# Optimization experiments

Measured on AMD Instinct MI355X. Metric: run time of the kernel, lower is better.

The kernel has to match this reference:

```python
import jax, jax.numpy as jnp
import numpy as np

LOG2E = 1.4426950408889634  # 1/ln(2): kernel works in log2 space with exp2


def _mlstm_chunkwise_single(q, k, v, vecI, vecF, chunk_size):
    # q,k: [T,K]; v: [T,V]; vecI,vecF: [T] (log2-space gate preactivations)
    T, K = q.shape
    V = v.shape[-1]
    BT = chunk_size
    NT = T // BT
    scale = K ** -0.5
    dt = q.dtype

    qc = q.reshape(NT, BT, K)
    kc = k.reshape(NT, BT, K)
    vc = v.reshape(NT, BT, V)
    ic = vecI.reshape(NT, BT)
    fc = vecF.reshape(NT, BT)
    b = jnp.cumsum(fc, axis=1)            # within-chunk cumulative log2 forget (vecF in kernel)
    f_last = b[:, -1]                      # scaF_last
    g = ic + f_last[:, None] - b           # decay from each pos to chunk end (vecG)

    tri = jnp.tril(jnp.ones((BT, BT), dtype=bool))

    def step(carry, inp):
        C, n, m = carry                    # [K,V], [K], scalar running max
        qt, kt, vt, it, bt, gt, fl = inp
        # intra-chunk decay matrix D[t,s] = i[s] + b[t] - b[s] for s<=t
        D = it[None, :] + bt[:, None] - bt[None, :]
        D = jnp.where(tri, D, -jnp.inf)
        m_intra = jnp.max(D, axis=1)                      # [BT]
        m_total = jnp.maximum(bt + m, m_intra)            # matM_total
        S = (qt @ kt.T) * (scale * jnp.exp2(D - m_total[:, None]))
        q_sc = qt * (scale * jnp.exp2(bt + m - m_total))[:, None]
        h_num = q_sc @ C + S @ vt                          # [BT,V]
        denom = jnp.maximum(jnp.abs(q_sc @ n + S.sum(axis=1)), jnp.exp2(-m_total))
        h = h_num / denom[:, None]
        # cross-chunk matrix-state recurrence with log2 restabilization
        m_next = jnp.maximum(fl + m, jnp.max(gt))
        dec = jnp.exp2(fl + m - m_next)
        kdec = kt * jnp.exp2(gt - m_next)[:, None]         # [BT,K]
        C_next = C * dec + kdec.T @ vt
        n_next = n * dec + kdec.sum(axis=0)
        return (C_next, n_next, m_next), h

    C0 = jnp.zeros((K, V), dt)
    n0 = jnp.zeros((K,), dt)
    m0 = jnp.zeros((), dt)
    _, hs = jax.lax.scan(step, (C0, n0, m0), (qc, kc, vc, ic, b, g, f_last))
    return hs.reshape(T, V)


def setup_inputs() -> dict:
    key = jax.random.key(0)
    ks = jax.random.split(key, 5)
    B, H, T, D = 8, 8, 4096, 64
    q = jax.random.normal(ks[0], (B, H, T, D), dtype=jnp.float32)
    k = jax.random.normal(ks[1], (B, H, T, D), dtype=jnp.float32)
    v = jax.random.normal(ks[2], (B, H, T, D), dtype=jnp.float32)
    i = jax.random.normal(ks[3], (B, H, T), dtype=jnp.float32)
    f = jax.random.normal(ks[4], (B, H, T), dtype=jnp.float32)
    return {"q": q, "k": k, "v": v, "i": i, "f": f, "chunk_size": 64}


def reference(q, k, v, i, f, chunk_size):
    B, H, T, K = q.shape
    V = v.shape[-1]
    vecF = jax.nn.log_sigmoid(f) * LOG2E   # log2 sigmoid(f)
    vecI = i * LOG2E                       # input gate in log2 space
    BH = B * H
    fn = lambda qq, kk, vv, ii, ff: _mlstm_chunkwise_single(qq, kk, vv, ii, ff, chunk_size)
    h = jax.vmap(fn)(q.reshape(BH, T, K), k.reshape(BH, T, K), v.reshape(BH, T, V),
                     vecI.reshape(BH, T), vecF.reshape(BH, T))
    return h.reshape(B, H, T, V)
```

## Files before the change

kernel.cpp:

```cpp
#include <hip/hip_runtime.h>
#include <hip/hip_bf16.h>
#include <math.h>

#define LOG2E_F 1.4426950408889634f

static constexpr int BT = 64;
static constexpr int DK = 64;
static constexpr int DV = 64;
static constexpr float SCALE = 0.125f;
static constexpr int PAD = 72;

typedef unsigned short ushort_t;
typedef __attribute__((ext_vector_type(8))) short short8;
typedef __attribute__((ext_vector_type(4))) float f32x4;
typedef __attribute__((ext_vector_type(4))) ushort_t ushort4v;

#define MFMA16(a, b, c) __builtin_amdgcn_mfma_f32_16x16x32_bf16((a), (b), (c), 0, 0, 0)

__device__ __forceinline__ int SWZ(int a, int b){ return a * PAD + (b ^ (((a >> 3) & 3) << 3)); }
__device__ __forceinline__ int ZSW(int r, int c){ return r * PAD + (c ^ (((r >> 2) & 3) << 3)); }
__device__ __forceinline__ int LIN(int r, int c){ return r * PAD + c; }

__device__ __forceinline__ float logsig_log2e(float x){
    float l = (x >= 0.f) ? (-log1pf(expf(-x))) : (x - log1pf(expf(x)));
    return l * LOG2E_F;
}
__device__ __forceinline__ ushort_t f2bf(float x){
    unsigned u = __builtin_bit_cast(unsigned, x);
    unsigned r = u + 0x7FFFu + ((u >> 16) & 1u);
    return (ushort_t)(r >> 16);
}
__device__ __forceinline__ float bf2f(ushort_t u){
    return __builtin_bit_cast(float, ((unsigned)u) << 16);
}
__device__ __forceinline__ void split_bf(float x, ushort_t& h, ushort_t& l){
    h = f2bf(x);
    l = f2bf(x - bf2f(h));
}

__global__ __launch_bounds__(256, 4) void stageA_kernel(
    const float* __restrict__ kg, const float* __restrict__ vg,
    const float* __restrict__ ig, const float* __restrict__ fg,
    float* __restrict__ A_ws, float* __restrict__ nloc_ws,
    float* __restrict__ fl_ws, float* __restrict__ mloc_ws,
    int T, int NT)
{
    const int ct = blockIdx.x, s = blockIdx.y, tid = threadIdx.x;
    const int w = tid >> 6, lane = tid & 63, ln = lane & 15, quad = lane >> 4;
    const int q8 = quad * 8;

    __shared__ __align__(16) ushort_t kth[BT * PAD];
    __shared__ __align__(16) ushort_t ktl[BT * PAD];
    __shared__ __align__(16) ushort_t vth[BT * PAD];
    __shared__ __align__(16) ushort_t vtl[BT * PAD];
    __shared__ float gsc[BT];

    const size_t rowbase = (size_t)s * T + (size_t)ct * BT;
    const float* kc = kg + rowbase * DK;
    const float* vc = vg + rowbase * DV;

    float4 kr[4], vr[4];
    #pragma unroll
    for (int i = 0; i < 4; ++i){
        int idx = i * 1024 + tid * 4;
        kr[i] = *(const float4*)(kc + idx);
        vr[i] = *(const float4*)(vc + idx);
    }
    if (tid < 64){
        float b = logsig_log2e(fg[rowbase + tid]);
        #pragma unroll
        for (int off = 1; off < 64; off <<= 1){
            float y = __shfl_up(b, off);
            if (tid >= off) b += y;
        }
        float f_last = __shfl(b, 63);
        float a = ig[rowbase + tid] * LOG2E_F - b;
        float p = a;
        #pragma unroll
        for (int off = 32; off > 0; off >>= 1) p = fmaxf(p, __shfl_xor(p, off));
        gsc[tid] = exp2f(a - p);
        if (tid == 0){ fl_ws[s * NT + ct] = f_last; mloc_ws[s * NT + ct] = f_last + p; }
    }
    __syncthreads();
    #pragma unroll
    for (int i = 0; i < 4; ++i){
        int idx = i * 1024 + tid * 4;
        int r = idx >> 6, c0 = idx & 63;
        float g = gsc[r];
        float kv[4] = {kr[i].x * g, kr[i].y * g, kr[i].z * g, kr[i].w * g};
        float vv[4] = {vr[i].x, vr[i].y, vr[i].z, vr[i].w};
        #pragma unroll
        for (int j = 0; j < 4; ++j){
            ushort_t h, l;
            split_bf(kv[j], h, l); kth[SWZ(c0 + j, r)] = h; ktl[SWZ(c0 + j, r)] = l;
            split_bf(vv[j], h, l); vth[SWZ(c0 + j, r)] = h; vtl[SWZ(c0 + j, r)] = l;
        }
    }
    __syncthreads();

    const int m = 16 * w + ln;
    short8 ah0 = *(const short8*)&kth[SWZ(m, q8)];
    short8 ah1 = *(const short8*)&kth[SWZ(m, 32 + q8)];
    short8 al0 = *(const short8*)&ktl[SWZ(m, q8)];
    short8 al1 = *(const short8*)&ktl[SWZ(m, 32 + q8)];
    float* Ab = A_ws + (size_t)(s * NT + ct) * 4096;
    #pragma unroll
    for (int t = 0; t < 4; ++t){
        f32x4 acc = {0.f, 0.f, 0.f, 0.f};
        short8 bh0 = *(const short8*)&vth[SWZ(16 * t + ln, q8)];
        short8 bh1 = *(const short8*)&vth[SWZ(16 * t + ln, 32 + q8)];
        short8 bl0 = *(const short8*)&vtl[SWZ(16 * t + ln, q8)];
        short8 bl1 = *(const short8*)&vtl[SWZ(16 * t + ln, 32 + q8)];
        acc = MFMA16(ah0, bh0, acc);
        acc = MFMA16(ah1, bh1, acc);
        acc = MFMA16(ah0, bl0, acc);
        acc = MFMA16(ah1, bl1, acc);
        acc = MFMA16(al0, bh0, acc);
        acc = MFMA16(al1, bh1, acc);
        *(f32x4*)(Ab + ((16 * t + ln) << 6) + 16 * w + quad * 4) = acc;
    }
    {
        short8 ones;
        #pragma unroll
        for (int j = 0; j < 8; ++j) ones[j] = (short)0x3F80;
        f32x4 nacc = {0.f, 0.f, 0.f, 0.f};
        nacc = MFMA16(ah0, ones, nacc);
        nacc = MFMA16(ah1, ones, nacc);
        nacc = MFMA16(al0, ones, nacc);
        nacc = MFMA16(al1, ones, nacc);
        if (ln == 0){
            #pragma unroll
            for (int reg = 0; reg < 4; ++reg)
                nloc_ws[((size_t)(s * NT + ct)) * DK + 16 * w + quad * 4 + reg] = nacc[reg];
        }
    }
}

__global__ __launch_bounds__(256) void stageB_kernel(
    const float* __restrict__ A_ws, const float* __restrict__ nloc_ws,
    const float* __restrict__ fl_ws, const float* __restrict__ mloc_ws,
    float* __restrict__ Cws, float* __restrict__ nws, float* __restrict__ mws,
    int NT)
{
    const int vb = blockIdx.x, s = blockIdx.y, tid = threadIdx.x;
    __shared__ float decs[64], scs[64];

    if (tid < 64){
        float fl = fl_ws[s * NT + tid];
        float ml = mloc_ws[s * NT + tid];
        float F = fl, G = ml;
        #pragma unroll
        for (int off = 1; off < 64; off <<= 1){
            float Fp = __shfl_up(F, off);
            float Gp = __shfl_up(G, off);
            if (tid >= off){ G = fmaxf(Gp + F, G); F = Fp + F; }
        }
        float m_next = fmaxf(F, G);
        float m_cur  = __shfl_up(m_next, 1);
        if (tid == 0) m_cur = 0.f;
        decs[tid] = exp2f(fl + m_cur - m_next);
        scs[tid]  = exp2f(ml - m_next);
        if (vb == 0) mws[s * NT + tid] = m_cur;
    }
    __syncthreads();

    const size_t base = (size_t)s * NT * 4096 + (size_t)vb * 256 + tid;
    const float* Ab = A_ws + base;
    float*       Cb = Cws  + base;
    const bool do_n = (vb == 0) && (tid < 64);

    float C = 0.f, nreg = 0.f;
    float p[8], nl[8];
    #pragma unroll
    for (int i = 0; i < 8; ++i){ p[i] = Ab[(size_t)i * 4096]; nl[i] = 0.f; }
    if (do_n){
        #pragma unroll
        for (int i = 0; i < 8; ++i) nl[i] = nloc_ws[((size_t)(s * NT + i)) * DK + tid];
    }

    for (int t0 = 0; t0 < NT; t0 += 8){
        float qv[8], nq[8];
        const int tn = t0 + 8;
        #pragma unroll
        for (int i = 0; i < 8; ++i)
            qv[i] = (tn + i < NT) ? Ab[(size_t)(tn + i) * 4096] : 0.f;
        #pragma unroll
        for (int i = 0; i < 8; ++i) nq[i] = 0.f;
        if (do_n){
            #pragma unroll
            for (int i = 0; i < 8; ++i)
                if (tn + i < NT) nq[i] = nloc_ws[((size_t)(s * NT + tn + i)) * DK + tid];
        }
        #pragma unroll
        for (int i = 0; i < 8; ++i){
            const int t = t0 + i;
            Cb[(size_t)t * 4096] = C;
            if (do_n) nws[((size_t)(s * NT + t)) * DK + tid] = nreg;
            const float d = decs[t], sc = scs[t];
            C = C * d + p[i] * sc;
            if (do_n) nreg = nreg * d + nl[i] * sc;
        }
        #pragma unroll
        for (int i = 0; i < 8; ++i){ p[i] = qv[i]; nl[i] = nq[i]; }
    }
}

__global__ __launch_bounds__(256, 4) void pass2_kernel(
    const float* __restrict__ qg, const float* __restrict__ kg, const float* __restrict__ vg,
    const float* __restrict__ ig, const float* __restrict__ fg,
    const float* __restrict__ Cws, const float* __restrict__ nws, const float* __restrict__ mws,
    float* __restrict__ out, int T, int NT)
{
    const int ct = blockIdx.x, s = blockIdx.y, tid = threadIdx.x;
    const int w = tid >> 6, lane = tid & 63, ln = lane & 15, quad = lane >> 4;
    const int q8 = quad * 8;

    __shared__ __align__(16) ushort_t bufA[BT * PAD];
    __shared__ __align__(16) ushort_t bufB[BT * PAD];
    __shared__ __align__(16) ushort_t bufZ[BT * PAD];
    __shared__ __align__(16) ushort_t bufV[BT * PAD];
    __shared__ float colterm[BT], Mr[BT], rowfac[BT], dncl[BT];
    __shared__ float nsh[DK], qn[BT], rowsum[BT];

    const size_t rowbase = (size_t)s * T + (size_t)ct * BT;
    const float* qc = qg + rowbase * DK;
    const float* kc = kg + rowbase * DK;
    const float* vc = vg + rowbase * DV;
    const float* Cc = Cws + ((size_t)(s * NT + ct)) * 4096;
    const float* nc = nws + ((size_t)(s * NT + ct)) * DK;
    const float m   = mws[s * NT + ct];

    float4 kr4[4], vr[4];
    #pragma unroll
    for (int i = 0; i < 4; ++i){
        int idx = i * 1024 + tid * 4;
        kr4[i] = *(const float4*)(kc + idx);
        vr[i]  = *(const float4*)(vc + idx);
    }
    const float* qrow = qc + (16 * w + ln) * DK;
    float4 qf0 = *(const float4*)(qrow + q8);
    float4 qf1 = *(const float4*)(qrow + q8 + 4);
    float4 qf2 = *(const float4*)(qrow + 32 + q8);
    float4 qf3 = *(const float4*)(qrow + 32 + q8 + 4);
    float4 Cr[4];
    #pragma unroll
    for (int i = 0; i < 4; ++i)
        Cr[i] = *(const float4*)(Cc + i * 1024 + tid * 4);

    if (tid < 64){
        float b = logsig_log2e(fg[rowbase + tid]);
        #pragma unroll
        for (int off = 1; off < 64; off <<= 1){
            float y = __shfl_up(b, off);
            if (tid >= off) b += y;
        }
        float a = ig[rowbase + tid] * LOG2E_F - b;
        float p = a;
        #pragma unroll
        for (int off = 1; off < 64; off <<= 1){
            float y = __shfl_up(p, off);
            if (tid >= off) p = fmaxf(p, y);
        }
        float M = fmaxf(m, p);
        colterm[tid] = a;
        Mr[tid] = M;
        rowfac[tid] = SCALE * exp2f(m - M);
        dncl[tid] = exp2f(-(b + M));
        nsh[tid] = nc[tid];
    }
    #pragma unroll
    for (int i = 0; i < 4; ++i){
        int idx = i * 1024 + tid * 4;
        int r = idx >> 6, c0 = idx & 63;
        float kv[4] = {kr4[i].x, kr4[i].y, kr4[i].z, kr4[i].w};
        ushort4v kh4, kl4;
        #pragma unroll
        for (int j = 0; j < 4; ++j){
            ushort_t h, l;
            split_bf(kv[j], h, l); kh4[j] = h; kl4[j] = l;
        }
        *(ushort4v*)&bufA[SWZ(r, c0)] = kh4;
        *(ushort4v*)&bufB[SWZ(r, c0)] = kl4;
    }
    __syncthreads();

    const int mrow = 16 * w + ln;
    float a0[8] = {qf0.x, qf0.y, qf0.z, qf0.w, qf1.x, qf1.y, qf1.z, qf1.w};
    float a1[8] = {qf2.x, qf2.y, qf2.z, qf2.w, qf3.x, qf3.y, qf3.z, qf3.w};
    short8 ah0, al0, ah1, al1;
    #pragma unroll
    for (int j = 0; j < 8; ++j){
        ushort_t h, l;
        split_bf(a0[j], h, l); ah0[j] = (short)h; al0[j] = (short)l;
        split_bf(a1[j], h, l); ah1[j] = (short)h; al1[j] = (short)l;
    }
    {
        float p = 0.f;
        #pragma unroll
        for (int j = 0; j < 8; ++j){
            p = fmaf(a0[j], nsh[q8 + j], p);
            p = fmaf(a1[j], nsh[32 + q8 + j], p);
        }
        p += __shfl_xor(p, 16);
        p += __shfl_xor(p, 32);
        if (quad == 0) qn[mrow] = p;
    }
    #pragma unroll
    for (int i = 0; i < 4; ++i){
        int idx = i * 1024 + tid * 4;
        int r = idx >> 6, c0 = idx & 63;
        float vv[4] = {vr[i].x, vr[i].y, vr[i].z, vr[i].w};
        #pragma unroll
        for (int j = 0; j < 4; ++j) bufV[SWZ(c0 + j, r)] = f2bf(vv[j]);
    }

    f32x4 sacc[4];
    #pragma unroll
    for (int t = 0; t < 4; ++t){
        sacc[t] = (f32x4){0.f, 0.f, 0.f, 0.f};
        short8 bh0 = *(const short8*)&bufA[SWZ(16 * t + ln, q8)];
        short8 bh1 = *(const short8*)&bufA[SWZ(16 * t + ln, 32 + q8)];
        short8 bl0 = *(const short8*)&bufB[SWZ(16 * t + ln, q8)];
        short8 bl1 = *(const short8*)&bufB[SWZ(16 * t + ln, 32 + q8)];
        sacc[t] = MFMA16(ah0, bh0, sacc[t]);
        sacc[t] = MFMA16(ah1, bh1, sacc[t]);
        sacc[t] = MFMA16(ah0, bl0, sacc[t]);
        sacc[t] = MFMA16(ah1, bl1, sacc[t]);
        sacc[t] = MFMA16(al0, bh0, sacc[t]);
        sacc[t] = MFMA16(al1, bh1, sacc[t]);
    }
    {
        float rsum[4] = {0.f, 0.f, 0.f, 0.f};
        float Mrv[4];
        #pragma unroll
        for (int reg = 0; reg < 4; ++reg) Mrv[reg] = Mr[16 * w + quad * 4 + reg];
        #pragma unroll
        for (int t = 0; t < 4; ++t){
            int c = 16 * t + ln;
            float cterm = colterm[c];
            #pragma unroll
            for (int reg = 0; reg < 4; ++reg){
                int r = 16 * w + quad * 4 + reg;
                float vS = (c <= r) ? sacc[t][reg] * SCALE * exp2f(cterm - Mrv[reg]) : 0.f;
                bufZ[ZSW(r, c)] = f2bf(vS);
                rsum[reg] += vS;
            }
        }
        #pragma unroll
        for (int off = 1; off < 16; off <<= 1){
            #pragma unroll
            for (int reg = 0; reg < 4; ++reg) rsum[reg] += __shfl_xor(rsum[reg], off);
        }
        if (ln == 0){
            #pragma unroll
            for (int reg = 0; reg < 4; ++reg) rowsum[16 * w + quad * 4 + reg] = rsum[reg];
        }
    }
    __syncthreads();

    #pragma unroll
    for (int i = 0; i < 4; ++i){
        int idx = i * 1024 + tid * 4;
        int vrow = idx >> 6, k0 = idx & 63;
        float cv[4] = {Cr[i].x, Cr[i].y, Cr[i].z, Cr[i].w};
        ushort4v ch4, cl4;
        #pragma unroll
        for (int j = 0; j < 4; ++j){
            ushort_t h, l;
            split_bf(cv[j], h, l); ch4[j] = h; cl4[j] = l;
        }
        *(ushort4v*)&bufA[SWZ(vrow, k0)] = ch4;
        *(ushort4v*)&bufB[SWZ(vrow, k0)] = cl4;
    }
    __syncthreads();

    f32x4 acc[4];
    #pragma unroll
    for (int t = 0; t < 4; ++t){
        acc[t] = (f32x4){0.f, 0.f, 0.f, 0.f};
        short8 bh0 = *(const short8*)&bufA[SWZ(16 * t + ln, q8)];
        short8 bh1 = *(const short8*)&bufA[SWZ(16 * t + ln, 32 + q8)];
        short8 bl0 = *(const short8*)&bufB[SWZ(16 * t + ln, q8)];
        short8 bl1 = *(const short8*)&bufB[SWZ(16 * t + ln, 32 + q8)];
        acc[t] = MFMA16(ah0, bh0, acc[t]);
        acc[t] = MFMA16(ah1, bh1, acc[t]);
        acc[t] = MFMA16(ah0, bl0, acc[t]);
        acc[t] = MFMA16(ah1, bl1, acc[t]);
        acc[t] = MFMA16(al0, bh0, acc[t]);
        acc[t] = MFMA16(al1, bh1, acc[t]);
    }
    float rf[4], inv[4];
    #pragma unroll
    for (int reg = 0; reg < 4; ++reg){
        int r = 16 * w + quad * 4 + reg;
        rf[reg] = rowfac[r];
        float dn = fabsf(rf[reg] * qn[r] + rowsum[r]);
        inv[reg] = 1.f / fmaxf(dn, dncl[r]);
    }
    #pragma unroll
    for (int t = 0; t < 4; ++t){
        #pragma unroll
        for (int reg = 0; reg < 4; ++reg) acc[t][reg] *= rf[reg];
    }
    short8 az0 = *(const short8*)&bufZ[ZSW(mrow, q8)];
    short8 az1 = *(const short8*)&bufZ[ZSW(mrow, 32 + q8)];
    #pragma unroll
    for (int t = 0; t < 4; ++t){
        short8 bh0 = *(const short8*)&bufV[SWZ(16 * t + ln, q8)];
        short8 bh1 = *(const short8*)&bufV[SWZ(16 * t + ln, 32 + q8)];
        acc[t] = MFMA16(az0, bh0, acc[t]);
        acc[t] = MFMA16(az1, bh1, acc[t]);
    }
    #pragma unroll
    for (int t = 0; t < 4; ++t){
        int c = 16 * t + ln;
        #pragma unroll
        for (int reg = 0; reg < 4; ++reg){
            int r = 16 * w + quad * 4 + reg;
            out[(rowbase + r) * DV + c] = acc[t][reg] * inv[reg];
        }
    }
}

__global__ __launch_bounds__(256) void fused_kernel(
    const float* __restrict__ qg, const float* __restrict__ kg, const float* __restrict__ vg,
    const float* __restrict__ ig, const float* __restrict__ fg,
    float* __restrict__ out, int T, int NT)
{
    const int s = blockIdx.x;
    const int tid = threadIdx.x;
    const int lane = tid & 63;

    __shared__ float X[BT][DK + 1];
    __shared__ float Y[BT][DK + 1];
    __shared__ float Cb[DK][DV];
    __shared__ __hip_bfloat16 Zh[BT][BT];
    __shared__ float colterm[BT], Mr[BT], rowfac[BT], dncl[BT], gscale[BT];
    __shared__ float nsh[DK], qn[BT], rowsum[BT], denom[BT];
    __shared__ float sh_dec;

    const float* qseq = qg + (size_t)s * T * DK;
    const float* kseq = kg + (size_t)s * T * DK;
    const float* vseq = vg + (size_t)s * T * DV;
    const float* iseq = ig + (size_t)s * T;
    const float* fseq = fg + (size_t)s * T;

    for (int idx = tid; idx < DK * DV; idx += 256) Cb[idx >> 6][idx & 63] = 0.f;
    if (tid < 64) nsh[lane] = 0.f;
    float m = 0.f;
    __syncthreads();

    const int r0 = (tid >> 4) * 4;
    const int c0 = (tid & 15) * 4;
    const int v0 = c0;

    for (int t = 0; t < NT; ++t){
        const size_t rb = (size_t)t * BT;
        if (tid < 64){
            float b = logsig_log2e(fseq[rb + lane]);
            #pragma unroll
            for (int off = 1; off < 64; off <<= 1){
                float y = __shfl_up(b, off);
                if (lane >= off) b += y;
            }
            float f_last = __shfl(b, 63);
            float a = iseq[rb + lane] * LOG2E_F - b;
            float p = a;
            #pragma unroll
            for (int off = 1; off < 64; off <<= 1){
                float y = __shfl_up(p, off);
                if (lane >= off) p = fmaxf(p, y);
            }
            float M = fmaxf(m, p);
            colterm[lane] = a;
            Mr[lane] = M;
            rowfac[lane] = SCALE * exp2f(m - M);
            dncl[lane] = exp2f(-(b + M));
            float g = a + f_last;
            float gm = g;
            #pragma unroll
            for (int off = 32; off > 0; off >>= 1) gm = fmaxf(gm, __shfl_xor(gm, off));
            float m_next = fmaxf(f_last + m, gm);
            gscale[lane] = exp2f(g - m_next);
            if (tid == 0) sh_dec = exp2f(f_last + m - m_next);
            m = m_next;
        }
        #pragma unroll
        for (int base = 0; base < BT * DK; base += 1024){
            int idx = base + tid * 4;
            int r = idx >> 6, c = idx & 63;
            float4 a4 = *(const float4*)(qseq + rb * DK + idx);
            X[r][c] = a4.x; X[r][c+1] = a4.y; X[r][c+2] = a4.z; X[r][c+3] = a4.w;
            float4 b4 = *(const float4*)(kseq + rb * DK + idx);
            Y[r][c] = b4.x; Y[r][c+1] = b4.y; Y[r][c+2] = b4.z; Y[r][c+3] = b4.w;
        }
        __syncthreads();

        float sacc[4][4] = {};
        for (int x = 0; x < DK; ++x){
            float xr[4], yc[4];
            #pragma unroll
            for (int j = 0; j < 4; ++j) xr[j] = X[r0 + j][x];
            #pragma unroll
            for (int j = 0; j < 4; ++j) yc[j] = Y[c0 + j][x];
            #pragma unroll
            for (int j = 0; j < 4; ++j)
                #pragma unroll
                for (int jj = 0; jj < 4; ++jj)
                    sacc[j][jj] = fmaf(xr[j], yc[jj], sacc[j][jj]);
        }
        float rs[4];
        #pragma unroll
        for (int j = 0; j < 4; ++j){
            int r = r0 + j;
            float Mrv = Mr[r];
            float acc = 0.f;
            #pragma unroll
            for (int jj = 0; jj < 4; ++jj){
                int c = c0 + jj;
                float vS = (c <= r) ? sacc[j][jj] * SCALE * exp2f(colterm[c] - Mrv) : 0.f;
                Zh[r][c] = __float2bfloat16(vS);
                acc += vS;
            }
            rs[j] = acc;
        }
        #pragma unroll
        for (int off = 1; off < 16; off <<= 1){
            #pragma unroll
            for (int j = 0; j < 4; ++j) rs[j] += __shfl_xor(rs[j], off);
        }
        if ((tid & 15) == 0){
            #pragma unroll
            for (int j = 0; j < 4; ++j) rowsum[r0 + j] = rs[j];
        }
        float acc1[4][4] = {};
        for (int x = 0; x < DK; ++x){
            float xr[4], yv[4];
            #pragma unroll
            for (int j = 0; j < 4; ++j) xr[j] = X[r0 + j][x];
            #pragma unroll
            for (int j = 0; j < 4; ++j) yv[j] = Cb[x][v0 + j];
            #pragma unroll
            for (int j = 0; j < 4; ++j)
                #pragma unroll
                for (int jj = 0; jj < 4; ++jj)
                    acc1[j][jj] = fmaf(xr[j], yv[jj], acc1[j][jj]);
        }
        if (tid < 64){
            float acc = 0.f;
            for (int x = 0; x < DK; ++x) acc = fmaf(X[lane][x], nsh[x], acc);
            qn[lane] = acc;
        }
        __syncthreads();

        #pragma unroll
        for (int base = 0; base < BT * DV; base += 1024){
            int idx = base + tid * 4;
            int r = idx >> 6, c = idx & 63;
            float4 a4 = *(const float4*)(vseq + rb * DV + idx);
            X[r][c] = a4.x; X[r][c+1] = a4.y; X[r][c+2] = a4.z; X[r][c+3] = a4.w;
        }
        if (tid < 64){
            float dn = fabsf(rowfac[lane] * qn[lane] + rowsum[lane]);
            denom[lane] = fmaxf(dn, dncl[lane]);
        }
        __syncthreads();

        float acc2[4][4] = {};
        for (int c = 0; c < BT; ++c){
            float zr[4], xv[4];
            #pragma unroll
            for (int j = 0; j < 4; ++j) zr[j] = __bfloat162float(Zh[r0 + j][c]);
            #pragma unroll
            for (int j = 0; j < 4; ++j) xv[j] = X[c][v0 + j];
            #pragma unroll
            for (int j = 0; j < 4; ++j)
                #pragma unroll
                for (int jj = 0; jj < 4; ++jj)
                    acc2[j][jj] = fmaf(zr[j], xv[jj], acc2[j][jj]);
        }
        #pragma unroll
        for (int j = 0; j < 4; ++j){
            int r = r0 + j;
            float rf = rowfac[r];
            float inv = 1.f / denom[r];
            float4 h4;
            h4.x = (acc1[j][0] * rf + acc2[j][0]) * inv;
            h4.y = (acc1[j][1] * rf + acc2[j][1]) * inv;
            h4.z = (acc1[j][2] * rf + acc2[j][2]) * inv;
            h4.w = (acc1[j][3] * rf + acc2[j][3]) * inv;
            *(float4*)(out + ((size_t)s * T + rb + r) * DV + v0) = h4;
        }
        {
            float dec = sh_dec;
            float cr[4][4];
            #pragma unroll
            for (int j = 0; j < 4; ++j)
                #pragma unroll
                for (int jj = 0; jj < 4; ++jj)
                    cr[j][jj] = Cb[r0 + j][c0 + jj] * dec;
            for (int c = 0; c < BT; ++c){
                float gs = gscale[c];
                float kd[4], xv[4];
                #pragma unroll
                for (int j = 0; j < 4; ++j) kd[j] = Y[c][r0 + j] * gs;
                #pragma unroll
                for (int jj = 0; jj < 4; ++jj) xv[jj] = X[c][c0 + jj];
                #pragma unroll
                for (int j = 0; j < 4; ++j)
                    #pragma unroll
                    for (int jj = 0; jj < 4; ++jj)
                        cr[j][jj] = fmaf(kd[j], xv[jj], cr[j][jj]);
            }
            #pragma unroll
            for (int j = 0; j < 4; ++j)
                #pragma unroll
                for (int jj = 0; jj < 4; ++jj)
                    Cb[r0 + j][c0 + jj] = cr[j][jj];
        }
        if (tid < 64){
            float acc = 0.f;
            for (int c = 0; c < BT; ++c) acc = fmaf(Y[c][lane], gscale[c], acc);
            nsh[lane] = nsh[lane] * sh_dec + acc;
        }
        __syncthreads();
    }
}

extern "C" void kernel_launch(void* const* d_in, const int* in_sizes, int n_in,
                              void* d_out, int out_size, void* d_ws, size_t ws_size,
                              hipStream_t stream)
{
    const float* q  = (const float*)d_in[0];
    const float* k  = (const float*)d_in[1];
    const float* v  = (const float*)d_in[2];
    const float* ii = (const float*)d_in[3];
    const float* ff = (const float*)d_in[4];
    float* out = (float*)d_out;

    const int T  = 4096;
    const int BH = in_sizes[3] / T;
    const int NT = T / BT;

    const size_t szC  = (size_t)BH * NT * DK * DV * sizeof(float);
    const size_t szA  = szC;
    const size_t szn  = (size_t)BH * NT * DK * sizeof(float);
    const size_t szs  = (size_t)BH * NT * sizeof(float);

    const size_t need_new = szA + szC + 2 * szn + 3 * szs;

    if (ws_size >= need_new){
        char* p = (char*)d_ws;
        float* A_ws    = (float*)p;            p += szA;
        float* Cws     = (float*)p;            p += szC;
        float* nloc_ws = (float*)p;            p += szn;
        float* nws     = (float*)p;            p += szn;
        float* fl_ws   = (float*)p;            p += szs;
        float* mloc_ws = (float*)p;            p += szs;
        float* mws     = (float*)p;
        stageA_kernel<<<dim3(NT, BH), 256, 0, stream>>>(k, v, ii, ff, A_ws, nloc_ws, fl_ws, mloc_ws, T, NT);
        stageB_kernel<<<dim3(16, BH), 256, 0, stream>>>(A_ws, nloc_ws, fl_ws, mloc_ws, Cws, nws, mws, NT);
        pass2_kernel<<<dim3(NT, BH), 256, 0, stream>>>(q, k, v, ii, ff, Cws, nws, mws, out, T, NT);
    } else {
        fused_kernel<<<dim3(BH), 256, 0, stream>>>(q, k, v, ii, ff, out, T, NT);
    }
}
```

Before: 292.1 us.

## Process four chunks per block with register prefetch of next chunk in stageA and pass2

Each block of stageA and pass2 now loops over four consecutive chunks instead of one. While the current chunk is being computed, the k, v, q, C, gate and state inputs for the next chunk are loaded into registers. The aim is to hide global load latency behind the MFMA work and to cut block launch count. In exchange the grid shrinks fourfold (4096 to 1024 blocks), register pressure rises from the prefetch buffers, and an extra barrier is added per chunk.

```diff
diff --git a/kernel.cpp b/kernel.cpp
--- a/kernel.cpp
+++ b/kernel.cpp
@@ -9,6 +9,7 @@
 static constexpr int DV = 64;
 static constexpr float SCALE = 0.125f;
 static constexpr int PAD = 72;
+static constexpr int CPB = 4;
 
 typedef unsigned short ushort_t;
 typedef __attribute__((ext_vector_type(8))) short short8;
@@ -45,9 +46,10 @@
     float* __restrict__ fl_ws, float* __restrict__ mloc_ws,
     int T, int NT)
 {
-    const int ct = blockIdx.x, s = blockIdx.y, tid = threadIdx.x;
+    const int cg = blockIdx.x, s = blockIdx.y, tid = threadIdx.x;
     const int w = tid >> 6, lane = tid & 63, ln = lane & 15, quad = lane >> 4;
     const int q8 = quad * 8;
+    const int ct0 = cg * CPB;
 
     __shared__ __align__(16) ushort_t kth[BT * PAD];
     __shared__ __align__(16) ushort_t ktl[BT * PAD];
@@ -55,83 +57,107 @@
     __shared__ __align__(16) ushort_t vtl[BT * PAD];
     __shared__ float gsc[BT];
 
-    const size_t rowbase = (size_t)s * T + (size_t)ct * BT;
-    const float* kc = kg + rowbase * DK;
-    const float* vc = vg + rowbase * DV;
-
+    size_t rowbase = (size_t)s * T + (size_t)ct0 * BT;
     float4 kr[4], vr[4];
     #pragma unroll
     for (int i = 0; i < 4; ++i){
         int idx = i * 1024 + tid * 4;
-        kr[i] = *(const float4*)(kc + idx);
-        vr[i] = *(const float4*)(vc + idx);
-    }
-    if (tid < 64){
-        float b = logsig_log2e(fg[rowbase + tid]);
-        #pragma unroll
-        for (int off = 1; off < 64; off <<= 1){
-            float y = __shfl_up(b, off);
-            if (tid >= off) b += y;
-        }
-        float f_last = __shfl(b, 63);
-        float a = ig[rowbase + tid] * LOG2E_F - b;
-        float p = a;
-        #pragma unroll
-        for (int off = 32; off > 0; off >>= 1) p = fmaxf(p, __shfl_xor(p, off));
-        gsc[tid] = exp2f(a - p);
-        if (tid == 0){ fl_ws[s * NT + ct] = f_last; mloc_ws[s * NT + ct] = f_last + p; }
-    }
-    __syncthreads();
+        kr[i] = *(const float4*)(kg + rowbase * DK + idx);
+        vr[i] = *(const float4*)(vg + rowbase * DV + idx);
+    }
+    float fv = 0.f, iv = 0.f;
+    if (tid < 64){ fv = fg[rowbase + tid]; iv = ig[rowbase + tid]; }
+
     #pragma unroll
-    for (int i = 0; i < 4; ++i){
-        int idx = i * 1024 + tid * 4;
-        int r = idx >> 6, c0 = idx & 63;
-        float g = gsc[r];
-        float kv[4] = {kr[i].x * g, kr[i].y * g, kr[i].z * g, kr[i].w * g};
-        float vv[4] = {vr[i].x, vr[i].y, vr[i].z, vr[i].w};
-        #pragma unroll
-        for (int j = 0; j < 4; ++j){
-            ushort_t h, l;
-            split_bf(kv[j], h, l); kth[SWZ(c0 + j, r)] = h; ktl[SWZ(c0 + j, r)] = l;
-            split_bf(vv[j], h, l); vth[SWZ(c0 + j, r)] = h; vtl[SWZ(c0 + j, r)] = l;
-        }
-    }
-    __syncthreads();
-
-    const int m = 16 * w + ln;
-    short8 ah0 = *(const short8*)&kth[SWZ(m, q8)];
-    short8 ah1 = *(const short8*)&kth[SWZ(m, 32 + q8)];
-    short8 al0 = *(const short8*)&ktl[SWZ(m, q8)];
-    short8 al1 = *(const short8*)&ktl[SWZ(m, 32 + q8)];
-    float* Ab = A_ws + (size_t)(s * NT + ct) * 4096;
-    #pragma unroll
-    for (int t = 0; t < 4; ++t){
-        f32x4 acc = {0.f, 0.f, 0.f, 0.f};
-        short8 bh0 = *(const short8*)&vth[SWZ(16 * t + ln, q8)];
-        short8 bh1 = *(const short8*)&vth[SWZ(16 * t + ln, 32 + q8)];
-        short8 bl0 = *(const short8*)&vtl[SWZ(16 * t + ln, q8)];
-        short8 bl1 = *(const short8*)&vtl[SWZ(16 * t + ln, 32 + q8)];
-        acc = MFMA16(ah0, bh0, acc);
-        acc = MFMA16(ah1, bh1, acc);
-        acc = MFMA16(ah0, bl0, acc);
-        acc = MFMA16(ah1, bl1, acc);
-        acc = MFMA16(al0, bh0, acc);
-        acc = MFMA16(al1, bh1, acc);
-        *(f32x4*)(Ab + ((16 * t + ln) << 6) + 16 * w + quad * 4) = acc;
-    }
-    {
-        short8 ones;
-        #pragma unroll
-        for (int j = 0; j < 8; ++j) ones[j] = (short)0x3F80;
-        f32x4 nacc = {0.f, 0.f, 0.f, 0.f};
-        nacc = MFMA16(ah0, ones, nacc);
-        nacc = MFMA16(ah1, ones, nacc);
-        nacc = MFMA16(al0, ones, nacc);
-        nacc = MFMA16(al1, ones, nacc);
-        if (ln == 0){
-            #pragma unroll
-            for (int reg = 0; reg < 4; ++reg)
-                nloc_ws[((size_t)(s * NT + ct)) * DK + 16 * w + quad * 4 + reg] = nacc[reg];
+    for (int c = 0; c < CPB; ++c){
+        const int ct = ct0 + c;
+        const size_t rb = (size_t)s * T + (size_t)ct * BT;
+
+        if (tid < 64){
+            float b = logsig_log2e(fv);
+            #pragma unroll
+            for (int off = 1; off < 64; off <<= 1){
+                float y = __shfl_up(b, off);
+                if (tid >= off) b += y;
+            }
+            float f_last = __shfl(b, 63);
+            float a = iv * LOG2E_F - b;
+            float p = a;
+            #pragma unroll
+            for (int off = 32; off > 0; off >>= 1) p = fmaxf(p, __shfl_xor(p, off));
+            gsc[tid] = exp2f(a - p);
+            if (tid == 0){ fl_ws[s * NT + ct] = f_last; mloc_ws[s * NT + ct] = f_last + p; }
+        }
+        float4 krn[4], vrn[4];
+        float fvn = 0.f, ivn = 0.f;
+        if (c + 1 < CPB){
+            const size_t rb2 = rb + BT;
+            #pragma unroll
+            for (int i = 0; i < 4; ++i){
+                int idx = i * 1024 + tid * 4;
+                krn[i] = *(const float4*)(kg + rb2 * DK + idx);
+                vrn[i] = *(const float4*)(vg + rb2 * DV + idx);
+            }
+            if (tid < 64){ fvn = fg[rb2 + tid]; ivn = ig[rb2 + tid]; }
+        }
+        __syncthreads();
+
+        #pragma unroll
+        for (int i = 0; i < 4; ++i){
+            int idx = i * 1024 + tid * 4;
+            int r = idx >> 6, c0 = idx & 63;
+            float g = gsc[r];
+            float kv[4] = {kr[i].x * g, kr[i].y * g, kr[i].z * g, kr[i].w * g};
+            float vv[4] = {vr[i].x, vr[i].y, vr[i].z, vr[i].w};
+            #pragma unroll
+            for (int j = 0; j < 4; ++j){
+                ushort_t h, l;
+                split_bf(kv[j], h, l); kth[SWZ(c0 + j, r)] = h; ktl[SWZ(c0 + j, r)] = l;
+                split_bf(vv[j], h, l); vth[SWZ(c0 + j, r)] = h; vtl[SWZ(c0 + j, r)] = l;
+            }
+        }
+        __syncthreads();
+
+        const int m = 16 * w + ln;
+        short8 ah0 = *(const short8*)&kth[SWZ(m, q8)];
+        short8 ah1 = *(const short8*)&kth[SWZ(m, 32 + q8)];
+        short8 al0 = *(const short8*)&ktl[SWZ(m, q8)];
+        short8 al1 = *(const short8*)&ktl[SWZ(m, 32 + q8)];
+        float* Ab = A_ws + (size_t)(s * NT + ct) * 4096;
+        #pragma unroll
+        for (int t = 0; t < 4; ++t){
+            f32x4 acc = {0.f, 0.f, 0.f, 0.f};
+            short8 bh0 = *(const short8*)&vth[SWZ(16 * t + ln, q8)];
+            short8 bh1 = *(const short8*)&vth[SWZ(16 * t + ln, 32 + q8)];
+            short8 bl0 = *(const short8*)&vtl[SWZ(16 * t + ln, q8)];
+            short8 bl1 = *(const short8*)&vtl[SWZ(16 * t + ln, 32 + q8)];
+            acc = MFMA16(ah0, bh0, acc);
+            acc = MFMA16(ah1, bh1, acc);
+            acc = MFMA16(ah0, bl0, acc);
+            acc = MFMA16(ah1, bl1, acc);
+            acc = MFMA16(al0, bh0, acc);
+            acc = MFMA16(al1, bh1, acc);
+            *(f32x4*)(Ab + ((16 * t + ln) << 6) + 16 * w + quad * 4) = acc;
+        }
+        {
+            short8 ones;
+            #pragma unroll
+            for (int j = 0; j < 8; ++j) ones[j] = (short)0x3F80;
+            f32x4 nacc = {0.f, 0.f, 0.f, 0.f};
+            nacc = MFMA16(ah0, ones, nacc);
+            nacc = MFMA16(ah1, ones, nacc);
+            nacc = MFMA16(al0, ones, nacc);
+            nacc = MFMA16(al1, ones, nacc);
+            if (ln == 0){
+                #pragma unroll
+                for (int reg = 0; reg < 4; ++reg)
+                    nloc_ws[((size_t)(s * NT + ct)) * DK + 16 * w + quad * 4 + reg] = nacc[reg];
+            }
+        }
+        if (c + 1 < CPB){
+            #pragma unroll
+            for (int i = 0; i < 4; ++i){ kr[i] = krn[i]; vr[i] = vrn[i]; }
+            fv = fvn; iv = ivn;
         }
     }
 }
@@ -211,9 +237,10 @@
     const float* __restrict__ Cws, const float* __restrict__ nws, const float* __restrict__ mws,
     float* __restrict__ out, int T, int NT)
 {
-    const int ct = blockIdx.x, s = blockIdx.y, tid = threadIdx.x;
+    const int cg = blockIdx.x, s = blockIdx.y, tid = threadIdx.x;
     const int w = tid >> 6, lane = tid & 63, ln = lane & 15, quad = lane >> 4;
     const int q8 = quad * 8;
+    const int ct0 = cg * CPB;
 
     __shared__ __align__(16) ushort_t bufA[BT * PAD];
     __shared__ __align__(16) ushort_t bufB[BT * PAD];
@@ -222,202 +249,245 @@
     __shared__ float colterm[BT], Mr[BT], rowfac[BT], dncl[BT];
     __shared__ float nsh[DK], qn[BT], rowsum[BT];
 
-    const size_t rowbase = (size_t)s * T + (size_t)ct * BT;
-    const float* qc = qg + rowbase * DK;
-    const float* kc = kg + rowbase * DK;
-    const float* vc = vg + rowbase * DV;
-    const float* Cc = Cws + ((size_t)(s * NT + ct)) * 4096;
-    const float* nc = nws + ((size_t)(s * NT + ct)) * DK;
-    const float m   = mws[s * NT + ct];
-
-    float4 kr4[4], vr[4];
+    {
+    }
+    size_t rb0 = (size_t)s * T + (size_t)ct0 * BT;
+    float4 kr4[4], vr[4], Cr[4], qf[4];
     #pragma unroll
     for (int i = 0; i < 4; ++i){
         int idx = i * 1024 + tid * 4;
-        kr4[i] = *(const float4*)(kc + idx);
-        vr[i]  = *(const float4*)(vc + idx);
-    }
-    const float* qrow = qc + (16 * w + ln) * DK;
-    float4 qf0 = *(const float4*)(qrow + q8);
-    float4 qf1 = *(const float4*)(qrow + q8 + 4);
-    float4 qf2 = *(const float4*)(qrow + 32 + q8);
-    float4 qf3 = *(const float4*)(qrow + 32 + q8 + 4);
-    float4 Cr[4];
+        kr4[i] = *(const float4*)(kg + rb0 * DK + idx);
+        vr[i]  = *(const float4*)(vg + rb0 * DV + idx);
+        Cr[i]  = *(const float4*)(Cws + ((size_t)(s * NT + ct0)) * 4096 + i * 1024 + tid * 4);
+    }
+    {
+        const float* qrow = qg + (rb0 + 16 * w + ln) * DK;
+        qf[0] = *(const float4*)(qrow + q8);
+        qf[1] = *(const float4*)(qrow + q8 + 4);
+        qf[2] = *(const float4*)(qrow + 32 + q8);
+        qf[3] = *(const float4*)(qrow + 32 + q8 + 4);
+    }
+    float fv = 0.f, iv = 0.f, nv = 0.f, mv = 0.f;
+    if (tid < 64){
+        fv = fg[rb0 + tid];
+        iv = ig[rb0 + tid];
+        nv = nws[((size_t)(s * NT + ct0)) * DK + tid];
+        mv = mws[s * NT + ct0];
+    }
+
     #pragma unroll
-    for (int i = 0; i < 4; ++i)
-        Cr[i] = *(const float4*)(Cc + i * 1024 + tid * 4);
-
-    if (tid < 64){
-        float b = logsig_log2e(fg[rowbase + tid]);
-        #pragma unroll
-        for (int off = 1; off < 64; off <<= 1){
-            float y = __shfl_up(b, off);
-            if (tid >= off) b += y;
-        }
-        float a = ig[rowbase + tid] * LOG2E_F - b;
-        float p = a;
-        #pragma unroll
-        for (int off = 1; off < 64; off <<= 1){
-            float y = __shfl_up(p, off);
-            if (tid >= off) p = fmaxf(p, y);
-        }
-        float M = fmaxf(m, p);
-        colterm[tid] = a;
-        Mr[tid] = M;
-        rowfac[tid] = SCALE * exp2f(m - M);
-        dncl[tid] = exp2f(-(b + M));
-        nsh[tid] = nc[tid];
-    }
-    #pragma unroll
-    for (int i = 0; i < 4; ++i){
-        int idx = i * 1024 + tid * 4;
-        int r = idx >> 6, c0 = idx & 63;
-        float kv[4] = {kr4[i].x, kr4[i].y, kr4[i].z, kr4[i].w};
-        ushort4v kh4, kl4;
-        #pragma unroll
-        for (int j = 0; j < 4; ++j){
+    for (int c = 0; c < CPB; ++c){
+        const int ct = ct0 + c;
+        const size_t rowbase = (size_t)s * T + (size_t)ct * BT;
+
+        if (tid < 64){
+            float b = logsig_log2e(fv);
+            #pragma unroll
+            for (int off = 1; off < 64; off <<= 1){
+                float y = __shfl_up(b, off);
+                if (tid >= off) b += y;
+            }
+            float a = iv * LOG2E_F - b;
+            float p = a;
+            #pragma unroll
+            for (int off = 1; off < 64; off <<= 1){
+                float y = __shfl_up(p, off);
+                if (tid >= off) p = fmaxf(p, y);
+            }
+            float M = fmaxf(mv, p);
+            colterm[tid] = a;
+            Mr[tid] = M;
+            rowfac[tid] = SCALE * exp2f(mv - M);
+            dncl[tid] = exp2f(-(b + M));
+            nsh[tid] = nv;
+        }
+        #pragma unroll
+        for (int i = 0; i < 4; ++i){
+            int idx = i * 1024 + tid * 4;
+            int r = idx >> 6, c0 = idx & 63;
+            float kv[4] = {kr4[i].x, kr4[i].y, kr4[i].z, kr4[i].w};
+            ushort4v kh4, kl4;
+            #pragma unroll
+            for (int j = 0; j < 4; ++j){
+                ushort_t h, l;
+                split_bf(kv[j], h, l); kh4[j] = h; kl4[j] = l;
+            }
+            *(ushort4v*)&bufA[SWZ(r, c0)] = kh4;
+            *(ushort4v*)&bufB[SWZ(r, c0)] = kl4;
+        }
+        float4 krn[4];
+        float fvn = 0.f, ivn = 0.f, nvn = 0.f, mvn = 0.f;
+        if (c + 1 < CPB){
+            const size_t rb2 = rowbase + BT;
+            #pragma unroll
+            for (int i = 0; i < 4; ++i)
+                krn[i] = *(const float4*)(kg + rb2 * DK + i * 1024 + tid * 4);
+            if (tid < 64){
+                fvn = fg[rb2 + tid];
+                ivn = ig[rb2 + tid];
+                nvn = nws[((size_t)(s * NT + ct + 1)) * DK + tid];
+                mvn = mws[s * NT + ct + 1];
+            }
+        }
+        __syncthreads();
+
+        const int mrow = 16 * w + ln;
+        float a0[8] = {qf[0].x, qf[0].y, qf[0].z, qf[0].w, qf[1].x, qf[1].y, qf[1].z, qf[1].w};
+        float a1[8] = {qf[2].x, qf[2].y, qf[2].z, qf[2].w, qf[3].x, qf[3].y, qf[3].z, qf[3].w};
+        short8 ah0, al0, ah1, al1;
+        #pragma unroll
+        for (int j = 0; j < 8; ++j){
             ushort_t h, l;
-            split_bf(kv[j], h, l); kh4[j] = h; kl4[j] = l;
-        }
-        *(ushort4v*)&bufA[SWZ(r, c0)] = kh4;
-        *(ushort4v*)&bufB[SWZ(r, c0)] = kl4;
-    }
-    __syncthreads();
-
-    const int mrow = 16 * w + ln;
-    float a0[8] = {qf0.x, qf0.y, qf0.z, qf0.w, qf1.x, qf1.y, qf1.z, qf1.w};
-    float a1[8] = {qf2.x, qf2.y, qf2.z, qf2.w, qf3.x, qf3.y, qf3.z, qf3.w};
-    short8 ah0, al0, ah1, al1;
-    #pragma unroll
-    for (int j = 0; j < 8; ++j){
-        ushort_t h, l;
-        split_bf(a0[j], h, l); ah0[j] = (short)h; al0[j] = (short)l;
-        split_bf(a1[j], h, l); ah1[j] = (short)h; al1[j] = (short)l;
-    }
-    {
-        float p = 0.f;
-        #pragma unroll
-        for (int j = 0; j < 8; ++j){
-            p = fmaf(a0[j], nsh[q8 + j], p);
-            p = fmaf(a1[j], nsh[32 + q8 + j], p);
-        }
-        p += __shfl_xor(p, 16);
-        p += __shfl_xor(p, 32);
-        if (quad == 0) qn[mrow] = p;
-    }
-    #pragma unroll
-    for (int i = 0; i < 4; ++i){
-        int idx = i * 1024 + tid * 4;
-        int r = idx >> 6, c0 = idx & 63;
-        float vv[4] = {vr[i].x, vr[i].y, vr[i].z, vr[i].w};
-        #pragma unroll
-        for (int j = 0; j < 4; ++j) bufV[SWZ(c0 + j, r)] = f2bf(vv[j]);
-    }
-
-    f32x4 sacc[4];
-    #pragma unroll
-    for (int t = 0; t < 4; ++t){
-        sacc[t] = (f32x4){0.f, 0.f, 0.f, 0.f};
-        short8 bh0 = *(const short8*)&bufA[SWZ(16 * t + ln, q8)];
-        short8 bh1 = *(const short8*)&bufA[SWZ(16 * t + ln, 32 + q8)];
-        short8 bl0 = *(const short8*)&bufB[SWZ(16 * t + ln, q8)];
-        short8 bl1 = *(const short8*)&bufB[SWZ(16 * t + ln, 32 + q8)];
-        sacc[t] = MFMA16(ah0, bh0, sacc[t]);
-        sacc[t] = MFMA16(ah1, bh1, sacc[t]);
-        sacc[t] = MFMA16(ah0, bl0, sacc[t]);
-        sacc[t] = MFMA16(ah1, bl1, sacc[t]);
-        sacc[t] = MFMA16(al0, bh0, sacc[t]);
-        sacc[t] = MFMA16(al1, bh1, sacc[t]);
-    }
-    {
-        float rsum[4] = {0.f, 0.f, 0.f, 0.f};
-        float Mrv[4];
-        #pragma unroll
-        for (int reg = 0; reg < 4; ++reg) Mrv[reg] = Mr[16 * w + quad * 4 + reg];
+            split_bf(a0[j], h, l); ah0[j] = (short)h; al0[j] = (short)l;
+            split_bf(a1[j], h, l); ah1[j] = (short)h; al1[j] = (short)l;
+        }
+        {
+            float p = 0.f;
+            #pragma unroll
+            for (int j = 0; j < 8; ++j){
+                p = fmaf(a0[j], nsh[q8 + j], p);
+                p = fmaf(a1[j], nsh[32 + q8 + j], p);
+            }
+            p += __shfl_xor(p, 16);
+            p += __shfl_xor(p, 32);
+            if (quad == 0) qn[mrow] = p;
+        }
+        #pragma unroll
+        for (int i = 0; i < 4; ++i){
+            int idx = i * 1024 + tid * 4;
+            int r = idx >> 6, c0 = idx & 63;
+            float vv[4] = {vr[i].x, vr[i].y, vr[i].z, vr[i].w};
+            #pragma unroll
+            for (int j = 0; j < 4; ++j) bufV[SWZ(c0 + j, r)] = f2bf(vv[j]);
+        }
+        f32x4 sacc[4];
         #pragma unroll
         for (int t = 0; t < 4; ++t){
-            int c = 16 * t + ln;
-            float cterm = colterm[c];
+            sacc[t] = (f32x4){0.f, 0.f, 0.f, 0.f};
+            short8 bh0 = *(const short8*)&bufA[SWZ(16 * t + ln, q8)];
+            short8 bh1 = *(const short8*)&bufA[SWZ(16 * t + ln, 32 + q8)];
+            short8 bl0 = *(const short8*)&bufB[SWZ(16 * t + ln, q8)];
+            short8 bl1 = *(const short8*)&bufB[SWZ(16 * t + ln, 32 + q8)];
+            sacc[t] = MFMA16(ah0, bh0, sacc[t]);
+            sacc[t] = MFMA16(ah1, bh1, sacc[t]);
+            sacc[t] = MFMA16(ah0, bl0, sacc[t]);
+            sacc[t] = MFMA16(ah1, bl1, sacc[t]);
+            sacc[t] = MFMA16(al0, bh0, sacc[t]);
+            sacc[t] = MFMA16(al1, bh1, sacc[t]);
+        }
+        {
+            float rsum[4] = {0.f, 0.f, 0.f, 0.f};
+            float Mrv[4];
+            #pragma unroll
+            for (int reg = 0; reg < 4; ++reg) Mrv[reg] = Mr[16 * w + quad * 4 + reg];
+            #pragma unroll
+            for (int t = 0; t < 4; ++t){
+                int cc = 16 * t + ln;
+                float cterm = colterm[cc];
+                #pragma unroll
+                for (int reg = 0; reg < 4; ++reg){
+                    int r = 16 * w + quad * 4 + reg;
+                    float vS = (cc <= r) ? sacc[t][reg] * SCALE * exp2f(cterm - Mrv[reg]) : 0.f;
+                    bufZ[ZSW(r, cc)] = f2bf(vS);
+                    rsum[reg] += vS;
+                }
+            }
+            #pragma unroll
+            for (int off = 1; off < 16; off <<= 1){
+                #pragma unroll
+                for (int reg = 0; reg < 4; ++reg) rsum[reg] += __shfl_xor(rsum[reg], off);
+            }
+            if (ln == 0){
+                #pragma unroll
+                for (int reg = 0; reg < 4; ++reg) rowsum[16 * w + quad * 4 + reg] = rsum[reg];
+            }
+        }
+        __syncthreads();
+
+        #pragma unroll
+        for (int i = 0; i < 4; ++i){
+            int idx = i * 1024 + tid * 4;
+            int vrow = idx >> 6, k0 = idx & 63;
+            float cv[4] = {Cr[i].x, Cr[i].y, Cr[i].z, Cr[i].w};
+            ushort4v ch4, cl4;
+            #pragma unroll
+            for (int j = 0; j < 4; ++j){
+                ushort_t h, l;
+                split_bf(cv[j], h, l); ch4[j] = h; cl4[j] = l;
+            }
+            *(ushort4v*)&bufA[SWZ(vrow, k0)] = ch4;
+            *(ushort4v*)&bufB[SWZ(vrow, k0)] = cl4;
+        }
+        float4 Crn[4], qfn[4], vrn[4];
+        if (c + 1 < CPB){
+            const size_t rb2 = rowbase + BT;
+            #pragma unroll
+            for (int i = 0; i < 4; ++i){
+                Crn[i] = *(const float4*)(Cws + ((size_t)(s * NT + ct + 1)) * 4096 + i * 1024 + tid * 4);
+                vrn[i] = *(const float4*)(vg + rb2 * DV + i * 1024 + tid * 4);
+            }
+            const float* qrow2 = qg + (rb2 + 16 * w + ln) * DK;
+            qfn[0] = *(const float4*)(qrow2 + q8);
+            qfn[1] = *(const float4*)(qrow2 + q8 + 4);
+            qfn[2] = *(const float4*)(qrow2 + 32 + q8);
+            qfn[3] = *(const float4*)(qrow2 + 32 + q8 + 4);
+        }
+        __syncthreads();
+
+        f32x4 acc[4];
+        #pragma unroll
+        for (int t = 0; t < 4; ++t){
+            acc[t] = (f32x4){0.f, 0.f, 0.f, 0.f};
+            short8 bh0 = *(const short8*)&bufA[SWZ(16 * t + ln, q8)];
+            short8 bh1 = *(const short8*)&bufA[SWZ(16 * t + ln, 32 + q8)];
+            short8 bl0 = *(const short8*)&bufB[SWZ(16 * t + ln, q8)];
+            short8 bl1 = *(const short8*)&bufB[SWZ(16 * t + ln, 32 + q8)];
+            acc[t] = MFMA16(ah0, bh0, acc[t]);
+            acc[t] = MFMA16(ah1, bh1, acc[t]);
+            acc[t] = MFMA16(ah0, bl0, acc[t]);
+            acc[t] = MFMA16(ah1, bl1, acc[t]);
+            acc[t] = MFMA16(al0, bh0, acc[t]);
+            acc[t] = MFMA16(al1, bh1, acc[t]);
+        }
+        float rf[4], inv[4];
+        #pragma unroll
+        for (int reg = 0; reg < 4; ++reg){
+            int r = 16 * w + quad * 4 + reg;
+            rf[reg] = rowfac[r];
+            float dn = fabsf(rf[reg] * qn[r] + rowsum[r]);
+            inv[reg] = 1.f / fmaxf(dn, dncl[r]);
+        }
+        #pragma unroll
+        for (int t = 0; t < 4; ++t){
+            #pragma unroll
+            for (int reg = 0; reg < 4; ++reg) acc[t][reg] *= rf[reg];
+        }
+        short8 az0 = *(const short8*)&bufZ[ZSW(mrow, q8)];
+        short8 az1 = *(const short8*)&bufZ[ZSW(mrow, 32 + q8)];
+        #pragma unroll
+        for (int t = 0; t < 4; ++t){
+            short8 bh0 = *(const short8*)&bufV[SWZ(16 * t + ln, q8)];
+            short8 bh1 = *(const short8*)&bufV[SWZ(16 * t + ln, 32 + q8)];
+            acc[t] = MFMA16(az0, bh0, acc[t]);
+            acc[t] = MFMA16(az1, bh1, acc[t]);
+        }
+        #pragma unroll
+        for (int t = 0; t < 4; ++t){
+            int cc = 16 * t + ln;
             #pragma unroll
             for (int reg = 0; reg < 4; ++reg){
                 int r = 16 * w + quad * 4 + reg;
-                float vS = (c <= r) ? sacc[t][reg] * SCALE * exp2f(cterm - Mrv[reg]) : 0.f;
-                bufZ[ZSW(r, c)] = f2bf(vS);
-                rsum[reg] += vS;
-            }
-        }
-        #pragma unroll
-        for (int off = 1; off < 16; off <<= 1){
-            #pragma unroll
-            for (int reg = 0; reg < 4; ++reg) rsum[reg] += __shfl_xor(rsum[reg], off);
-        }
-        if (ln == 0){
-            #pragma unroll
-            for (int reg = 0; reg < 4; ++reg) rowsum[16 * w + quad * 4 + reg] = rsum[reg];
-        }
-    }
-    __syncthreads();
-
-    #pragma unroll
-    for (int i = 0; i < 4; ++i){
-        int idx = i * 1024 + tid * 4;
-        int vrow = idx >> 6, k0 = idx & 63;
-        float cv[4] = {Cr[i].x, Cr[i].y, Cr[i].z, Cr[i].w};
-        ushort4v ch4, cl4;
-        #pragma unroll
-        for (int j = 0; j < 4; ++j){
-            ushort_t h, l;
-            split_bf(cv[j], h, l); ch4[j] = h; cl4[j] = l;
-        }
-        *(ushort4v*)&bufA[SWZ(vrow, k0)] = ch4;
-        *(ushort4v*)&bufB[SWZ(vrow, k0)] = cl4;
-    }
-    __syncthreads();
-
-    f32x4 acc[4];
-    #pragma unroll
-    for (int t = 0; t < 4; ++t){
-        acc[t] = (f32x4){0.f, 0.f, 0.f, 0.f};
-        short8 bh0 = *(const short8*)&bufA[SWZ(16 * t + ln, q8)];
-        short8 bh1 = *(const short8*)&bufA[SWZ(16 * t + ln, 32 + q8)];
-        short8 bl0 = *(const short8*)&bufB[SWZ(16 * t + ln, q8)];
-        short8 bl1 = *(const short8*)&bufB[SWZ(16 * t + ln, 32 + q8)];
-        acc[t] = MFMA16(ah0, bh0, acc[t]);
-        acc[t] = MFMA16(ah1, bh1, acc[t]);
-        acc[t] = MFMA16(ah0, bl0, acc[t]);
-        acc[t] = MFMA16(ah1, bl1, acc[t]);
-        acc[t] = MFMA16(al0, bh0, acc[t]);
-        acc[t] = MFMA16(al1, bh1, acc[t]);
-    }
-    float rf[4], inv[4];
-    #pragma unroll
-    for (int reg = 0; reg < 4; ++reg){
-        int r = 16 * w + quad * 4 + reg;
-        rf[reg] = rowfac[r];
-        float dn = fabsf(rf[reg] * qn[r] + rowsum[r]);
-        inv[reg] = 1.f / fmaxf(dn, dncl[r]);
-    }
-    #pragma unroll
-    for (int t = 0; t < 4; ++t){
-        #pragma unroll
-        for (int reg = 0; reg < 4; ++reg) acc[t][reg] *= rf[reg];
-    }
-    short8 az0 = *(const short8*)&bufZ[ZSW(mrow, q8)];
-    short8 az1 = *(const short8*)&bufZ[ZSW(mrow, 32 + q8)];
-    #pragma unroll
-    for (int t = 0; t < 4; ++t){
-        short8 bh0 = *(const short8*)&bufV[SWZ(16 * t + ln, q8)];
-        short8 bh1 = *(const short8*)&bufV[SWZ(16 * t + ln, 32 + q8)];
-        acc[t] = MFMA16(az0, bh0, acc[t]);
-        acc[t] = MFMA16(az1, bh1, acc[t]);
-    }
-    #pragma unroll
-    for (int t = 0; t < 4; ++t){
-        int c = 16 * t + ln;
-        #pragma unroll
-        for (int reg = 0; reg < 4; ++reg){
-            int r = 16 * w + quad * 4 + reg;
-            out[(rowbase + r) * DV + c] = acc[t][reg] * inv[reg];
+                out[(rowbase + r) * DV + cc] = acc[t][reg] * inv[reg];
+            }
+        }
+
+        if (c + 1 < CPB){
+            __syncthreads();
+            #pragma unroll
+            for (int i = 0; i < 4; ++i){
+                kr4[i] = krn[i]; Cr[i] = Crn[i]; qf[i] = qfn[i]; vr[i] = vrn[i];
+            }
+            fv = fvn; iv = ivn; nv = nvn; mv = mvn;
         }
     }
 }
@@ -649,7 +719,7 @@
 
     const size_t need_new = szA + szC + 2 * szn + 3 * szs;
 
-    if (ws_size >= need_new){
+    if (ws_size >= need_new && (NT % CPB) == 0){
         char* p = (char*)d_ws;
         float* A_ws    = (float*)p;            p += szA;
         float* Cws     = (float*)p;            p += szC;
@@ -658,9 +728,9 @@
         float* fl_ws   = (float*)p;            p += szs;
         float* mloc_ws = (float*)p;            p += szs;
         float* mws     = (float*)p;
-        stageA_kernel<<<dim3(NT, BH), 256, 0, stream>>>(k, v, ii, ff, A_ws, nloc_ws, fl_ws, mloc_ws, T, NT);
+        stageA_kernel<<<dim3(NT / CPB, BH), 256, 0, stream>>>(k, v, ii, ff, A_ws, nloc_ws, fl_ws, mloc_ws, T, NT);
         stageB_kernel<<<dim3(16, BH), 256, 0, stream>>>(A_ws, nloc_ws, fl_ws, mloc_ws, Cws, nws, mws, NT);
-        pass2_kernel<<<dim3(NT, BH), 256, 0, stream>>>(q, k, v, ii, ff, Cws, nws, mws, out, T, NT);
+        pass2_kernel<<<dim3(NT / CPB, BH), 256, 0, stream>>>(q, k, v, ii, ff, Cws, nws, mws, out, T, NT);
     } else {
         fused_kernel<<<dim3(BH), 256, 0, stream>>>(q, k, v, ii, ff, out, T, NT);
     }
```

Result: slower. 379.2 us (+29.8%).
